# Optimization experiments

Hardware: AMD Instinct MI355X
Metric: run time of the kernel (lower is better)

The kernel has to match this reference:

```python
import jax, jax.numpy as jnp
import numpy as np

N_NODES = 100000
N_RELS = 4
N_EDGES = 200000
D_IN = 256
D_OUT = 256
N_BASES = 2
LN_EPS = 1e-5


def setup_inputs() -> dict:
    key = jax.random.key(0)
    ks = jax.random.split(key, 8)
    x = jax.random.normal(ks[0], (N_NODES, D_IN), dtype=jnp.float32)
    src_idx = jax.random.randint(ks[1], (N_RELS, N_EDGES), 0, N_NODES, dtype=jnp.int32)
    dst_idx = jax.random.randint(ks[2], (N_RELS, N_EDGES), 0, N_NODES, dtype=jnp.int32)
    # WeightBasis: bases [B, in, out], per-relation coefficients [R, B]
    xav = float(np.sqrt(2.0)) * float(np.sqrt(6.0 / (D_IN + D_OUT)))
    bases = jax.random.uniform(ks[3], (N_BASES, D_IN, D_OUT), minval=-xav, maxval=xav, dtype=jnp.float32)
    w_comp = jax.random.normal(ks[4], (N_RELS, N_BASES), dtype=jnp.float32) * 0.5
    loop_weight = jax.random.uniform(ks[5], (D_IN, D_OUT), minval=-xav, maxval=xav, dtype=jnp.float32)
    h_bias = jnp.zeros((D_OUT,), dtype=jnp.float32)
    ln_gamma = jnp.ones((D_OUT,), dtype=jnp.float32)
    ln_beta = jnp.zeros((D_OUT,), dtype=jnp.float32)
    return {"x": x, "src_idx": src_idx, "dst_idx": dst_idx, "bases": bases,
            "w_comp": w_comp, "loop_weight": loop_weight, "h_bias": h_bias,
            "ln_gamma": ln_gamma, "ln_beta": ln_beta}


def reference(x, src_idx, dst_idx, bases, w_comp, loop_weight, h_bias, ln_gamma, ln_beta):
    n = x.shape[0]
    # basis combination -> per-relation weights [R, in, out]
    W = jnp.einsum('rb,bio->rio', w_comp, bases)

    def per_rel(W_r, s, d):
        # GraphConv(norm='right', weight=W_r): aggregate src feats to dst,
        # normalize by in-degree (clamped to 1), then matmul.
        msgs = x[s]                                            # [E, in]
        agg = jax.ops.segment_sum(msgs, d, num_segments=n)     # [N, in]
        deg = jax.ops.segment_sum(jnp.ones(d.shape, x.dtype), d, num_segments=n)
        agg = agg / jnp.maximum(deg, 1.0)[:, None]
        return agg @ W_r                                        # [N, out]

    hs = jax.vmap(per_rel)(W, src_idx, dst_idx).sum(axis=0)    # HeteroGraphConv sum aggregate
    # self-loop + bias
    h = hs + x @ loop_weight + h_bias
    # layer norm
    mu = jnp.mean(h, axis=-1, keepdims=True)
    var = jnp.mean(jnp.square(h - mu), axis=-1, keepdims=True)
    h = (h - mu) * jax.lax.rsqrt(var + LN_EPS) * ln_gamma + ln_beta
    # activation (dropout inactive in eval; NGNN has 0 layers)
    return jax.nn.relu(h)
```

## Files before the change

kernel.cpp:

```cpp
#include <hip/hip_runtime.h>


#define NN 100000
#define NR 4
#define NE 200000
#define CAP 32
#define BM 128

typedef __attribute__((ext_vector_type(8))) short short8;
typedef __attribute__((ext_vector_type(16))) float floatx16;

__device__ __forceinline__ unsigned short f2bf(float f) {
  unsigned u = __float_as_uint(f);
  u += 0x7FFFu + ((u >> 16) & 1u);
  return (unsigned short)(u >> 16);
}

__global__ void prep(const float* __restrict__ x, const float* __restrict__ bases,
                     const float* __restrict__ loop_w, const int* __restrict__ src,
                     const int* __restrict__ dst, unsigned short* __restrict__ Xbf,
                     unsigned short* __restrict__ Bfrag, int* __restrict__ cnt,
                     int* __restrict__ edgebuf) {
  const int b = blockIdx.x;
  const int tid = threadIdx.x;
  if (b < 12500) {
    int i = b * 256 + tid;
    int row = i >> 5;
    int col = (i & 31) << 3;
    const float4 v0 = *(const float4*)(x + (size_t)row * 256 + col);
    const float4 v1 = *(const float4*)(x + (size_t)row * 256 + col + 4);
    uint4 u;
    u.x = (unsigned)f2bf(v0.x) | ((unsigned)f2bf(v0.y) << 16);
    u.y = (unsigned)f2bf(v0.z) | ((unsigned)f2bf(v0.w) << 16);
    u.z = (unsigned)f2bf(v1.x) | ((unsigned)f2bf(v1.y) << 16);
    u.w = (unsigned)f2bf(v1.z) | ((unsigned)f2bf(v1.w) << 16);
    *(uint4*)(Xbf + (size_t)row * 256 + col) = u;
  } else if (b < 13268) {
    int i = (b - 12500) * 256 + tid;
    int e = i & 7;
    int lane = (i >> 3) & 63;
    int f = i >> 9;
    int t = f & 7;
    int j = (f >> 3) & 7;
    int s = f >> 6;
    int n = t * 32 + (lane & 31);
    int k = s * 128 + j * 16 + (lane >> 5) * 8 + e;
    float v;
    if (k < 256)      v = bases[k * 256 + n];
    else if (k < 512) v = bases[65536 + (k - 256) * 256 + n];
    else              v = loop_w[(k - 512) * 256 + n];
    Bfrag[i] = f2bf(v);
  } else {
    int i = (b - 13268) * 256 + tid;
    int r = i / NE;
    int s = src[i];
    int dd = dst[i];
    int pos = atomicAdd(&cnt[dd], 1);
    if (pos < CAP) edgebuf[dd * CAP + pos] = s | (r << 20);
  }
}

__global__ void agg_edges(const int* __restrict__ edgebuf, const int* __restrict__ cnt,
                          const float* __restrict__ w_comp,
                          const unsigned short* __restrict__ Xbf,
                          unsigned short* __restrict__ Cp) {
  const int tid = threadIdx.x;
  const int lane = tid & 63;
  const int wave = tid >> 6;
  const int half = lane >> 5;
  const int l31 = lane & 31;
  const int d = blockIdx.x * 8 + wave * 2 + half;

  int cc = cnt[d]; cc = cc < CAP ? cc : CAP;
  int ev = 0;
  if (l31 < cc) ev = edgebuf[d * CAP + l31];
  const int rl = ev >> 20;

  unsigned long long b0 = __ballot((l31 < cc) && rl == 0);
  unsigned long long b1 = __ballot((l31 < cc) && rl == 1);
  unsigned long long b2 = __ballot((l31 < cc) && rl == 2);
  unsigned long long b3 = __ballot((l31 < cc) && rl == 3);
  const int sh = half << 5;
  float i0 = 1.0f / fmaxf((float)__popc((unsigned)(b0 >> sh)), 1.0f);
  float i1 = 1.0f / fmaxf((float)__popc((unsigned)(b1 >> sh)), 1.0f);
  float i2 = 1.0f / fmaxf((float)__popc((unsigned)(b2 >> sh)), 1.0f);
  float i3 = 1.0f / fmaxf((float)__popc((unsigned)(b3 >> sh)), 1.0f);
  float s00 = w_comp[0] * i0, s10 = w_comp[1] * i0;
  float s01 = w_comp[2] * i1, s11 = w_comp[3] * i1;
  float s02 = w_comp[4] * i2, s12 = w_comp[5] * i2;
  float s03 = w_comp[6] * i3, s13 = w_comp[7] * i3;

  float a0[8] = {0.f, 0.f, 0.f, 0.f, 0.f, 0.f, 0.f, 0.f};
  float a1[8] = {0.f, 0.f, 0.f, 0.f, 0.f, 0.f, 0.f, 0.f};
  const unsigned short* Xp = Xbf + l31 * 8;
  const int selbase = lane & 32;

#define EDGE_W(v, w0, w1)                                            \
  int r_##w0 = (v) >> 20;                                            \
  float w0 = r_##w0 < 2 ? (r_##w0 == 0 ? s00 : s01)                  \
                        : (r_##w0 == 2 ? s02 : s03);                 \
  float w1 = r_##w0 < 2 ? (r_##w0 == 0 ? s10 : s11)                  \
                        : (r_##w0 == 2 ? s12 : s13);

#define ACC8(g, w0, w1)                                              \
  {                                                                  \
    float e0 = __uint_as_float((g).x << 16);                         \
    float e1 = __uint_as_float((g).x & 0xFFFF0000u);                 \
    float e2 = __uint_as_float((g).y << 16);                         \
    float e3 = __uint_as_float((g).y & 0xFFFF0000u);                 \
    float e4 = __uint_as_float((g).z << 16);                         \
    float e5 = __uint_as_float((g).z & 0xFFFF0000u);                 \
    float e6 = __uint_as_float((g).w << 16);                         \
    float e7 = __uint_as_float((g).w & 0xFFFF0000u);                 \
    a0[0] += (w0) * e0; a0[1] += (w0) * e1; a0[2] += (w0) * e2;      \
    a0[3] += (w0) * e3; a0[4] += (w0) * e4; a0[5] += (w0) * e5;      \
    a0[6] += (w0) * e6; a0[7] += (w0) * e7;                          \
    a1[0] += (w1) * e0; a1[1] += (w1) * e1; a1[2] += (w1) * e2;      \
    a1[3] += (w1) * e3; a1[4] += (w1) * e4; a1[5] += (w1) * e5;      \
    a1[6] += (w1) * e6; a1[7] += (w1) * e7;                          \
  }

  int i = 0;
  for (; i + 4 <= cc; i += 4) {
    int v0 = __shfl(ev, selbase + i);
    int v1 = __shfl(ev, selbase + i + 1);
    int v2 = __shfl(ev, selbase + i + 2);
    int v3 = __shfl(ev, selbase + i + 3);
    const uint4 g0 = *(const uint4*)(Xp + (size_t)(v0 & 0xFFFFF) * 256);
    const uint4 g1 = *(const uint4*)(Xp + (size_t)(v1 & 0xFFFFF) * 256);
    const uint4 g2 = *(const uint4*)(Xp + (size_t)(v2 & 0xFFFFF) * 256);
    const uint4 g3 = *(const uint4*)(Xp + (size_t)(v3 & 0xFFFFF) * 256);
    { EDGE_W(v0, w0a, w1a) ACC8(g0, w0a, w1a) }
    { EDGE_W(v1, w0b, w1b) ACC8(g1, w0b, w1b) }
    { EDGE_W(v2, w0c, w1c) ACC8(g2, w0c, w1c) }
    { EDGE_W(v3, w0d, w1d) ACC8(g3, w0d, w1d) }
  }
  for (; i < cc; ++i) {
    int v = __shfl(ev, selbase + i);
    const uint4 g = *(const uint4*)(Xp + (size_t)(v & 0xFFFFF) * 256);
    EDGE_W(v, w0, w1)
    ACC8(g, w0, w1)
  }

  uint4 o0, o1;
  o0.x = (unsigned)f2bf(a0[0]) | ((unsigned)f2bf(a0[1]) << 16);
  o0.y = (unsigned)f2bf(a0[2]) | ((unsigned)f2bf(a0[3]) << 16);
  o0.z = (unsigned)f2bf(a0[4]) | ((unsigned)f2bf(a0[5]) << 16);
  o0.w = (unsigned)f2bf(a0[6]) | ((unsigned)f2bf(a0[7]) << 16);
  o1.x = (unsigned)f2bf(a1[0]) | ((unsigned)f2bf(a1[1]) << 16);
  o1.y = (unsigned)f2bf(a1[2]) | ((unsigned)f2bf(a1[3]) << 16);
  o1.z = (unsigned)f2bf(a1[4]) | ((unsigned)f2bf(a1[5]) << 16);
  o1.w = (unsigned)f2bf(a1[6]) | ((unsigned)f2bf(a1[7]) << 16);
  *(uint4*)(Cp + (size_t)d * 512 + l31 * 8) = o0;
  *(uint4*)(Cp + (size_t)d * 512 + 256 + l31 * 8) = o1;
}

__launch_bounds__(256, 2)
__global__ void gemm_ln(const unsigned short* __restrict__ Cp,
                        const unsigned short* __restrict__ Xbf,
                        const unsigned short* __restrict__ Bfrag,
                        const float* __restrict__ h_bias, const float* __restrict__ gamma,
                        const float* __restrict__ beta, float* __restrict__ out) {
  const int tid = threadIdx.x;
  const int wave = tid >> 6;
  const int lane = tid & 63;
  const int l31 = lane & 31;
  const int half = lane >> 5;
  const int m0 = blockIdx.x * BM;

  floatx16 acc[8];
#pragma unroll
  for (int t = 0; t < 8; ++t)
#pragma unroll
    for (int r = 0; r < 16; ++r) acc[t][r] = 0.0f;

  int arow = m0 + wave * 32 + l31;
  if (arow >= NN) arow = NN - 1;
  const unsigned short* gC = Cp + (size_t)arow * 512 + half * 8;
  const unsigned short* gX = Xbf + (size_t)arow * 256 + half * 8;
  const unsigned short* gB = Bfrag + lane * 8;

  short8 Af[2][8];
  short8 Bf[2][8];

#pragma unroll
  for (int j = 0; j < 8; ++j) Af[0][j] = *(const short8*)(gC + j * 16);
#pragma unroll
  for (int t = 0; t < 8; ++t) Bf[0][t] = *(const short8*)(gB + t * 512);

#pragma unroll
  for (int s = 0; s < 6; ++s) {
    if (s < 5) {
      const unsigned short* ap =
          (s + 1 < 4) ? gC + (s + 1) * 128 : gX + (s + 1 - 4) * 128;
#pragma unroll
      for (int j = 0; j < 8; ++j)
        Af[(s + 1) & 1][j] = *(const short8*)(ap + j * 16);
    }
#pragma unroll
    for (int j = 0; j < 8; ++j) {
      const int cur = j & 1;
      if (!(s == 5 && j == 7)) {
        const int ns = (j == 7) ? s + 1 : s;
        const int nj = (j + 1) & 7;
        const unsigned short* bp = gB + (size_t)(ns * 8 + nj) * 8 * 512;
#pragma unroll
        for (int t = 0; t < 8; ++t)
          Bf[cur ^ 1][t] = *(const short8*)(bp + t * 512);
      }
      short8 af = Af[s & 1][j];
#pragma unroll
      for (int t = 0; t < 8; ++t)
        acc[t] = __builtin_amdgcn_mfma_f32_32x32x16_bf16(af, Bf[cur][t], acc[t], 0, 0, 0);
    }
  }

  float bcol[8], gc[8], bc[8];
#pragma unroll
  for (int t = 0; t < 8; ++t) {
    int col = t * 32 + l31;
    bcol[t] = h_bias[col];
    gc[t] = gamma[col];
    bc[t] = beta[col];
  }
#pragma unroll
  for (int t = 0; t < 8; ++t)
#pragma unroll
    for (int r = 0; r < 16; ++r) acc[t][r] += bcol[t];

  const int m_base = m0 + wave * 32;
#pragma unroll
  for (int r = 0; r < 16; ++r) {
    float s = 0.f, q = 0.f;
#pragma unroll
    for (int t = 0; t < 8; ++t) { float v = acc[t][r]; s += v; q += v * v; }
#pragma unroll
    for (int m = 16; m >= 1; m >>= 1) {
      s += __shfl_xor(s, m);
      q += __shfl_xor(q, m);
    }
    float mean = s * (1.0f / 256.0f);
    float var = q * (1.0f / 256.0f) - mean * mean;
    float rstd = rsqrtf(var + 1e-5f);
    int row = (r & 3) + ((r >> 2) << 3) + (half << 2);
    int grow = m_base + row;
    if (grow < NN) {
#pragma unroll
      for (int t = 0; t < 8; ++t) {
        float v = (acc[t][r] - mean) * rstd * gc[t] + bc[t];
        out[(size_t)grow * 256 + t * 32 + l31] = fmaxf(v, 0.0f);
      }
    }
  }
}

extern "C" void kernel_launch(void* const* d_in, const int* in_sizes, int n_in,
                              void* d_out, int out_size, void* d_ws, size_t ws_size,
                              hipStream_t stream) {
  const float* x      = (const float*)d_in[0];
  const int*   src    = (const int*)d_in[1];
  const int*   dst    = (const int*)d_in[2];
  const float* bases  = (const float*)d_in[3];
  const float* w_comp = (const float*)d_in[4];
  const float* loop_w = (const float*)d_in[5];
  const float* h_bias = (const float*)d_in[6];
  const float* gamma  = (const float*)d_in[7];
  const float* beta   = (const float*)d_in[8];
  float* out = (float*)d_out;

  char* ws = (char*)d_ws;
  unsigned short* Cp    = (unsigned short*)ws;
  unsigned short* Xbf   = (unsigned short*)(ws + 102400000);
  unsigned short* Bfrag = (unsigned short*)(ws + 153600000);
  int* cnt     = (int*)(ws + 153993216);
  int* edgebuf = (int*)(ws + 154393216);

  hipMemsetAsync(cnt, 0, 400000, stream);

  prep<<<16393, 256, 0, stream>>>(x, bases, loop_w, src, dst, Xbf, Bfrag, cnt, edgebuf);
  agg_edges<<<12500, 256, 0, stream>>>(edgebuf, cnt, w_comp, Xbf, Cp);
  gemm_ln<<<(NN + BM - 1) / BM, 256, 0, stream>>>(Cp, Xbf, Bfrag, h_bias, gamma, beta, out);
}
```

Baseline: 432.8 us.

## Stage GEMM A/B tiles through LDS via async global_load_lds double buffering

Replaces the register-prefetch operand loading in the fused GEMM+LayerNorm kernel with direct global-to-LDS asynchronous loads (global_load_lds, 16 bytes per lane) into double-buffered shared tiles. Each block now loads a shared B fragment tile once per k-step instead of every wave reading B separately from global memory, and uses __syncthreads per stage. It adds 48KB of LDS per block and a barrier per step, which may limit occupancy and pipelining.

```diff
diff --git a/kernel.cpp b/kernel.cpp
--- a/kernel.cpp
+++ b/kernel.cpp
@@ -14,6 +14,12 @@
   unsigned u = __float_as_uint(f);
   u += 0x7FFFu + ((u >> 16) & 1u);
   return (unsigned short)(u >> 16);
+}
+
+__device__ __forceinline__ void gload16(const unsigned short* g, unsigned short* l) {
+  __builtin_amdgcn_global_load_lds(
+      (const __attribute__((address_space(1))) unsigned int*)g,
+      (__attribute__((address_space(3))) unsigned int*)l, 16, 0, 0);
 }
 
 __global__ void prep(const float* __restrict__ x, const float* __restrict__ bases,
@@ -161,6 +167,8 @@
                         const unsigned short* __restrict__ Bfrag,
                         const float* __restrict__ h_bias, const float* __restrict__ gamma,
                         const float* __restrict__ beta, float* __restrict__ out) {
+  __shared__ unsigned short Ab[2][128 * 32];
+  __shared__ unsigned short Bb[2][256 * 32];
   const int tid = threadIdx.x;
   const int wave = tid >> 6;
   const int lane = tid & 63;
@@ -174,45 +182,44 @@
 #pragma unroll
     for (int r = 0; r < 16; ++r) acc[t][r] = 0.0f;
 
-  int arow = m0 + wave * 32 + l31;
+  int arow = m0 + 32 * wave + l31;
   if (arow >= NN) arow = NN - 1;
-  const unsigned short* gC = Cp + (size_t)arow * 512 + half * 8;
-  const unsigned short* gX = Xbf + (size_t)arow * 256 + half * 8;
-  const unsigned short* gB = Bfrag + lane * 8;
-
-  short8 Af[2][8];
-  short8 Bf[2][8];
-
-#pragma unroll
-  for (int j = 0; j < 8; ++j) Af[0][j] = *(const short8*)(gC + j * 16);
-#pragma unroll
-  for (int t = 0; t < 8; ++t) Bf[0][t] = *(const short8*)(gB + t * 512);
-
-#pragma unroll
-  for (int s = 0; s < 6; ++s) {
-    if (s < 5) {
-      const unsigned short* ap =
-          (s + 1 < 4) ? gC + (s + 1) * 128 : gX + (s + 1 - 4) * 128;
-#pragma unroll
-      for (int j = 0; j < 8; ++j)
-        Af[(s + 1) & 1][j] = *(const short8*)(ap + j * 16);
+  const unsigned short* pC0 = Cp + (size_t)arow * 512 + half * 8;
+  const unsigned short* pC1 = pC0 + 16;
+  const unsigned short* pX0 = Xbf + (size_t)arow * 256 + half * 8;
+  const unsigned short* pX1 = pX0 + 16;
+  const unsigned short* pB = Bfrag + tid * 8;
+
+#define STAGE(s, buf)                                                     \
+  {                                                                       \
+    const int ks = (s) * 32;                                              \
+    const unsigned short* a0 = ((s) < 16) ? pC0 + ks : pX0 + ks - 512;    \
+    const unsigned short* a1 = ((s) < 16) ? pC1 + ks : pX1 + ks - 512;    \
+    gload16(a0, &Ab[buf][(wave * 2 + 0) * 64 * 8] + lane * 8);            \
+    gload16(a1, &Ab[buf][(wave * 2 + 1) * 64 * 8] + lane * 8);            \
+    const unsigned short* bsrc = pB + (size_t)(s) * 8192;                 \
+    gload16(bsrc,        &Bb[buf][0]    + tid * 8);                       \
+    gload16(bsrc + 2048, &Bb[buf][2048] + tid * 8);                       \
+    gload16(bsrc + 4096, &Bb[buf][4096] + tid * 8);                       \
+    gload16(bsrc + 6144, &Bb[buf][6144] + tid * 8);                       \
+  }
+
+  STAGE(0, 0)
+  __syncthreads();
+
+  for (int s = 0; s < 24; ++s) {
+    const int cur = s & 1;
+    if (s < 23) STAGE(s + 1, cur ^ 1)
+#pragma unroll
+    for (int j = 0; j < 2; ++j) {
+      short8 af = *(const short8*)(&Ab[cur][(wave * 2 + j) * 512] + lane * 8);
+#pragma unroll
+      for (int t = 0; t < 8; ++t) {
+        short8 bfr = *(const short8*)(&Bb[cur][(j * 8 + t) * 512] + lane * 8);
+        acc[t] = __builtin_amdgcn_mfma_f32_32x32x16_bf16(af, bfr, acc[t], 0, 0, 0);
+      }
     }
-#pragma unroll
-    for (int j = 0; j < 8; ++j) {
-      const int cur = j & 1;
-      if (!(s == 5 && j == 7)) {
-        const int ns = (j == 7) ? s + 1 : s;
-        const int nj = (j + 1) & 7;
-        const unsigned short* bp = gB + (size_t)(ns * 8 + nj) * 8 * 512;
-#pragma unroll
-        for (int t = 0; t < 8; ++t)
-          Bf[cur ^ 1][t] = *(const short8*)(bp + t * 512);
-      }
-      short8 af = Af[s & 1][j];
-#pragma unroll
-      for (int t = 0; t < 8; ++t)
-        acc[t] = __builtin_amdgcn_mfma_f32_32x32x16_bf16(af, Bf[cur][t], acc[t], 0, 0, 0);
-    }
+    __syncthreads();
   }
 
   float bcol[8], gc[8], bc[8];
```

Measured after the change: 382.5 us. -11.6%, faster.
